# Performance work log

Hardware: AMD Instinct MI355X
Metric: run time of the kernel (lower is better)

The kernel has to match this reference:

```python
import jax, jax.numpy as jnp
import numpy as np

B, T, N, D, E = 16, 12, 512, 128, 32  # batch, time, nodes, model_dim, node_emb_dim


def setup_inputs() -> dict:
    key = jax.random.key(0)
    ks = jax.random.split(key, 7)
    return {
        "value": jax.random.normal(ks[0], (B, T, N, D), dtype=jnp.float32),
        "emb": jax.random.normal(ks[1], (T, N, E), dtype=jnp.float32),
        "attn_mask": jax.random.randint(ks[2], (B, N, N), 0, 2, dtype=jnp.int32),
        "W_qk": jax.random.normal(ks[3], (E, D), dtype=jnp.float32) * (1.0 / np.sqrt(E)),
        "b_qk": jax.random.normal(ks[4], (D,), dtype=jnp.float32) * 0.02,
        "W_v": jax.random.normal(ks[5], (D, D), dtype=jnp.float32) * (1.0 / np.sqrt(D)),
        "b_v": jax.random.normal(ks[6], (D,), dtype=jnp.float32) * 0.02,
    }


def reference(value, emb, attn_mask, W_qk, b_qk, W_v, b_v):
    # qk projection shared between query and key: [T, N, D]
    qk = emb @ W_qk + b_qk
    # query: softmax over feature dim D
    q = jax.nn.softmax(qk, axis=-1)                      # [T, N, D]
    # key: transpose then softmax over node dim N
    k = jax.nn.softmax(jnp.swapaxes(qk, -1, -2), axis=-1)  # [T, D, N]
    # value projection (note: out_proj in __init__ is unused in forward)
    v = value @ W_v + b_v                                # [B, T, N, D]
    # batch-independent base attention score, then broadcast over batch
    score = jnp.einsum('tnd,tdm->tnm', q, k)             # [T, N, N]
    score = jnp.broadcast_to(score[None], (value.shape[0],) + score.shape)  # [B, T, N, N]
    # masked fill: mask [B, N, N] -> [B, 1, N, N]
    score = jnp.where(attn_mask[:, None] == 0, jnp.float32(-1e9), score)
    out = jnp.einsum('btnm,btmd->btnd', score, v)         # [B, T, N, D]
    return out
```

## Files before the change

kernel.cpp:

```cpp
#include <hip/hip_runtime.h>

#define B_ 16
#define T_ 12
#define N_ 512
#define D_ 128
#define E_ 32

typedef __attribute__((ext_vector_type(8))) unsigned short u16x8;
typedef __attribute__((ext_vector_type(8))) __bf16 bf16x8;
typedef __attribute__((ext_vector_type(4))) float f32x4;

static __device__ __forceinline__ unsigned short f2bf(float f) {
    unsigned u = __float_as_uint(f);
    unsigned r = (u + 0x7fffu + ((u >> 16) & 1u)) >> 16;
    return (unsigned short)r;
}

static __device__ __forceinline__ void gld16(const void* src, void* dst) {
    __builtin_amdgcn_global_load_lds(
        (const __attribute__((address_space(1))) unsigned*)src,
        (__attribute__((address_space(3))) unsigned*)dst, 16, 0, 0);
}

__global__ __launch_bounds__(256) void k1(const float* __restrict__ emb,
                                          const float* __restrict__ Wqk,
                                          const float* __restrict__ bqk,
                                          unsigned short* __restrict__ qb,
                                          unsigned short* __restrict__ kN,
                                          const float* __restrict__ Wv,
                                          unsigned short* __restrict__ WvT,
                                          const int* __restrict__ mask,
                                          unsigned* __restrict__ mb) {
    __shared__ __align__(16) char LE[256 * 128];
    __shared__ float red[2][4][8];
    int bid = blockIdx.x;
    int tid = threadIdx.x;

    if (bid < 192) {
        int t = bid >> 4;
        int d0 = (bid & 15) * 8;
        int dc = tid & 7, ni = tid >> 3;
        float wqv[E_];
#pragma unroll
        for (int e = 0; e < E_; ++e) wqv[e] = Wqk[e * D_ + d0 + dc];
        float bq = bqk[d0 + dc];
        const float4* eb4 = (const float4*)(emb + (size_t)t * N_ * E_);

        float4 st0[8], st1[8];
#pragma unroll
        for (int ii = 0; ii < 8; ++ii) st0[ii] = eb4[ii * 256 + tid];
#pragma unroll
        for (int ii = 0; ii < 8; ++ii) {
            int f = ii * 256 + tid;
            int n = f >> 3, s = f & 7;
            *(float4*)(LE + n * 128 + ((s * 16) ^ ((n & 7) << 4))) = st0[ii];
        }
#pragma unroll
        for (int ii = 0; ii < 8; ++ii) st1[ii] = eb4[2048 + ii * 256 + tid];
        __syncthreads();

        float vals[16];
#pragma unroll
        for (int jj = 0; jj < 8; ++jj) {
            int n = ni + 32 * jj;
            float a = bq;
#pragma unroll
            for (int s = 0; s < 8; ++s) {
                f32x4 ev = *(const f32x4*)(LE + n * 128 + ((s * 16) ^ ((n & 7) << 4)));
                a = fmaf(ev[0], wqv[s * 4 + 0], a);
                a = fmaf(ev[1], wqv[s * 4 + 1], a);
                a = fmaf(ev[2], wqv[s * 4 + 2], a);
                a = fmaf(ev[3], wqv[s * 4 + 3], a);
            }
            vals[jj] = a;
        }
        __syncthreads();
#pragma unroll
        for (int ii = 0; ii < 8; ++ii) {
            int f = ii * 256 + tid;
            int n = f >> 3, s = f & 7;
            *(float4*)(LE + n * 128 + ((s * 16) ^ ((n & 7) << 4))) = st1[ii];
        }
        __syncthreads();
#pragma unroll
        for (int jj = 0; jj < 8; ++jj) {
            int n = ni + 32 * jj;
            float a = bq;
#pragma unroll
            for (int s = 0; s < 8; ++s) {
                f32x4 ev = *(const f32x4*)(LE + n * 128 + ((s * 16) ^ ((n & 7) << 4)));
                a = fmaf(ev[0], wqv[s * 4 + 0], a);
                a = fmaf(ev[1], wqv[s * 4 + 1], a);
                a = fmaf(ev[2], wqv[s * 4 + 2], a);
                a = fmaf(ev[3], wqv[s * 4 + 3], a);
            }
            vals[8 + jj] = a;
        }

        float mx = -1e30f;
#pragma unroll
        for (int j = 0; j < 16; ++j) mx = fmaxf(mx, vals[j]);
#pragma unroll
        for (int s = 8; s < 64; s <<= 1) mx = fmaxf(mx, __shfl_xor(mx, s));
        int wv = tid >> 6;
        if ((tid & 63) < 8) red[0][wv][dc] = mx;
        __syncthreads();
        mx = fmaxf(fmaxf(red[0][0][dc], red[0][1][dc]),
                   fmaxf(red[0][2][dc], red[0][3][dc]));
        float sum = 0.f;
#pragma unroll
        for (int j = 0; j < 16; ++j) {
            vals[j] = __expf(vals[j] - mx);
            sum += vals[j];
        }
#pragma unroll
        for (int s = 8; s < 64; s <<= 1) sum += __shfl_xor(sum, s);
        if ((tid & 63) < 8) red[1][wv][dc] = sum;
        __syncthreads();
        sum = red[1][0][dc] + red[1][1][dc] + red[1][2][dc] + red[1][3][dc];
        float inv = 1.f / sum;
        unsigned short* op = kN + (size_t)t * N_ * D_ + d0 + dc;
#pragma unroll
        for (int j = 0; j < 16; ++j)
            op[(size_t)(ni + 32 * j) * D_] = f2bf(vals[j] * inv);
        return;
    }

    if (bid < 576) {
        int bid2 = bid - 192;
        int w = tid >> 6, l = tid & 63;
        float wq0[E_], wq1[E_];
#pragma unroll
        for (int e = 0; e < E_; ++e) {
            wq0[e] = Wqk[e * D_ + l];
            wq1[e] = Wqk[e * D_ + l + 64];
        }
        float b0 = bqk[l], b1 = bqk[l + 64];
        for (int rr = 0; rr < 4; ++rr) {
            int tn = bid2 * 16 + w * 4 + rr;
            const float* ep = emb + (size_t)tn * E_;
            float a0 = b0, a1 = b1;
#pragma unroll
            for (int e = 0; e < E_; ++e) {
                float ev = ep[e];
                a0 = fmaf(ev, wq0[e], a0);
                a1 = fmaf(ev, wq1[e], a1);
            }
            float mx = fmaxf(a0, a1);
#pragma unroll
            for (int s = 32; s > 0; s >>= 1) mx = fmaxf(mx, __shfl_xor(mx, s));
            float e0 = __expf(a0 - mx), e1 = __expf(a1 - mx);
            float sum = e0 + e1;
#pragma unroll
            for (int s = 32; s > 0; s >>= 1) sum += __shfl_xor(sum, s);
            float inv = 1.f / sum;
            qb[(size_t)tn * D_ + l] = f2bf(e0 * inv);
            qb[(size_t)tn * D_ + l + 64] = f2bf(e1 * inv);
        }
        return;
    }

    if (bid < 1088) {
        int o = (bid - 576) * 256 + tid;
        const int* mp = mask + (size_t)o * 32;
        unsigned bits = 0;
#pragma unroll
        for (int j = 0; j < 32; j += 4) {
            int4 m4 = *(const int4*)&mp[j];
            bits |= (m4.x ? 1u : 0u) << j;
            bits |= (m4.y ? 1u : 0u) << (j + 1);
            bits |= (m4.z ? 1u : 0u) << (j + 2);
            bits |= (m4.w ? 1u : 0u) << (j + 3);
        }
        mb[o] = bits;
        return;
    }

    {
        int i = (bid - 1088) * 256 + tid;
        int d = i >> 7, k = i & 127;
        WvT[d * 128 + k] = f2bf(Wv[k * 128 + d]);
    }
}

__global__ __launch_bounds__(256, 2) void kF(const unsigned short* __restrict__ qb,
                                             const unsigned short* __restrict__ kN,
                                             unsigned short* __restrict__ sc,
                                             const float* __restrict__ value,
                                             const unsigned short* __restrict__ WvT,
                                             const float* __restrict__ bv,
                                             unsigned short* __restrict__ vT) {
    __shared__ __align__(16) char LA[2][128 * 128];
    __shared__ __align__(16) char LB[2][128 * 128];
    int bid = blockIdx.x;
    int tid = threadIdx.x;
    int wave = tid >> 6, lane = tid & 63;
    int q = lane >> 4, lr = lane & 15;
    int rbase = (wave & 1) * 64, cbase = (wave >> 1) * 64;
    int l3 = lane >> 3, l7 = lane & 7;

    f32x4 acc[4][4];
#pragma unroll
    for (int i = 0; i < 4; ++i)
#pragma unroll
        for (int j = 0; j < 4; ++j) acc[i][j] = (f32x4){0.f, 0.f, 0.f, 0.f};

#define STAGE_T(gbase, lb, c)                                                   \
    _Pragma("unroll") for (int it_ = 0; it_ < 4; ++it_) {                       \
        int row_ = it_ * 32 + wave * 8 + l3;                                    \
        gld16((gbase) + (size_t)row_ * 256 + (c) * 128 +                        \
                  ((l7 * 16) ^ ((row_ & 7) << 4)),                              \
              (lb) + (it_ * 32 + wave * 8) * 128 + lane * 16);                  \
    }

#define MFMA_CHUNK(c)                                                           \
    _Pragma("unroll") for (int ksl_ = 0; ksl_ < 2; ++ksl_) {                    \
        bf16x8 a_[4], b_[4];                                                    \
        _Pragma("unroll") for (int i_ = 0; i_ < 4; ++i_) {                      \
            int r_ = rbase + 16 * i_ + lr;                                      \
            a_[i_] = *(const bf16x8*)(LA[c] + r_ * 128 +                        \
                                      ((ksl_ * 64 + q * 16) ^ ((r_ & 7) << 4)));\
        }                                                                       \
        _Pragma("unroll") for (int j_ = 0; j_ < 4; ++j_) {                      \
            int r_ = cbase + 16 * j_ + lr;                                      \
            b_[j_] = *(const bf16x8*)(LB[c] + r_ * 128 +                        \
                                      ((ksl_ * 64 + q * 16) ^ ((r_ & 7) << 4)));\
        }                                                                       \
        _Pragma("unroll") for (int i_ = 0; i_ < 4; ++i_)                        \
            _Pragma("unroll") for (int j_ = 0; j_ < 4; ++j_)                    \
                acc[i_][j_] = __builtin_amdgcn_mfma_f32_16x16x32_bf16(          \
                    a_[i_], b_[j_], acc[i_][j_], 0, 0, 0);                      \
    }

    if (bid < 192) {
        int mt = bid & 3, nt = (bid >> 2) & 3, t = bid >> 4;
        int n0 = nt * 128, m0 = mt * 128;
        const char* qp = (const char*)(qb + (size_t)t * N_ * D_ + (size_t)n0 * D_);
        const char* kp = (const char*)(kN + (size_t)t * N_ * D_ + (size_t)m0 * D_);
        STAGE_T(qp, LA[0], 0)
        STAGE_T(kp, LB[0], 0)
        STAGE_T(qp, LA[1], 1)
        STAGE_T(kp, LB[1], 1)
        asm volatile("s_waitcnt vmcnt(8)" ::: "memory");
        __builtin_amdgcn_sched_barrier(0);
        __builtin_amdgcn_s_barrier();
        __builtin_amdgcn_sched_barrier(0);
        MFMA_CHUNK(0)
        asm volatile("s_waitcnt vmcnt(0)" ::: "memory");
        __builtin_amdgcn_sched_barrier(0);
        __builtin_amdgcn_s_barrier();
        __builtin_amdgcn_sched_barrier(0);
        MFMA_CHUNK(1)

        unsigned short* sp = sc + (size_t)t * N_ * N_;
#pragma unroll
        for (int i = 0; i < 4; ++i)
#pragma unroll
            for (int j = 0; j < 4; ++j) {
                int row0 = n0 + rbase + 16 * i + q * 4;
                int col = m0 + cbase + 16 * j + lr;
#pragma unroll
                for (int e = 0; e < 4; ++e)
                    sp[(size_t)(row0 + e) * N_ + col] = f2bf(acc[i][j][e]);
            }
        return;
    }

    {
        int idx = bid - 192;
        int mt = idx & 3, bt = idx >> 2;
        int m0 = mt * 128;
        const float* vp = value + ((size_t)bt * N_ + m0) * D_;
        const char* wp = (const char*)WvT;
        int g = tid >> 4, c16 = tid & 15;

        float4 v0[8], v1[8];
#pragma unroll
        for (int jj = 0; jj < 8; ++jj)
            v0[jj] = *(const float4*)(vp + (size_t)(g * 8 + jj) * D_ + c16 * 4);
        __builtin_amdgcn_sched_barrier(0);
        STAGE_T(wp, LA[0], 0)
        __builtin_amdgcn_sched_barrier(0);
#pragma unroll
        for (int jj = 0; jj < 8; ++jj)
            v1[jj] = *(const float4*)(vp + (size_t)(g * 8 + jj) * D_ + 64 + c16 * 4);
        __builtin_amdgcn_sched_barrier(0);
        STAGE_T(wp, LA[1], 1)
        __builtin_amdgcn_sched_barrier(0);

#pragma unroll
        for (int jj = 0; jj < 8; ++jj) {
            int row = g * 8 + jj;
            ushort4 o;
            o.x = f2bf(v0[jj].x); o.y = f2bf(v0[jj].y);
            o.z = f2bf(v0[jj].z); o.w = f2bf(v0[jj].w);
            *(ushort4*)(LB[0] + row * 128 + ((c16 * 8) ^ ((row & 7) << 4))) = o;
        }
        asm volatile("s_waitcnt vmcnt(12) lgkmcnt(0)" ::: "memory");
        __builtin_amdgcn_sched_barrier(0);
        __builtin_amdgcn_s_barrier();
        __builtin_amdgcn_sched_barrier(0);
        MFMA_CHUNK(0)
#pragma unroll
        for (int jj = 0; jj < 8; ++jj) {
            int row = g * 8 + jj;
            ushort4 o;
            o.x = f2bf(v1[jj].x); o.y = f2bf(v1[jj].y);
            o.z = f2bf(v1[jj].z); o.w = f2bf(v1[jj].w);
            *(ushort4*)(LB[1] + row * 128 + ((c16 * 8) ^ ((row & 7) << 4))) = o;
        }
        asm volatile("s_waitcnt vmcnt(0) lgkmcnt(0)" ::: "memory");
        __builtin_amdgcn_sched_barrier(0);
        __builtin_amdgcn_s_barrier();
        __builtin_amdgcn_sched_barrier(0);
        MFMA_CHUNK(1)

        unsigned short* op = vT + (size_t)bt * N_ * D_;
#pragma unroll
        for (int i = 0; i < 4; ++i) {
            int row0 = rbase + 16 * i + q * 4;
            float4 bq = *(const float4*)&bv[row0];
#pragma unroll
            for (int j = 0; j < 4; ++j) {
                int col = m0 + cbase + 16 * j + lr;
                op[(size_t)(row0 + 0) * N_ + col] = f2bf(acc[i][j][0] + bq.x);
                op[(size_t)(row0 + 1) * N_ + col] = f2bf(acc[i][j][1] + bq.y);
                op[(size_t)(row0 + 2) * N_ + col] = f2bf(acc[i][j][2] + bq.z);
                op[(size_t)(row0 + 3) * N_ + col] = f2bf(acc[i][j][3] + bq.w);
            }
        }
    }
#undef STAGE_T
#undef MFMA_CHUNK
}

__global__ __launch_bounds__(256, 3) void kC(const unsigned short* __restrict__ sc,
                                             const unsigned* __restrict__ mb,
                                             const unsigned short* __restrict__ vT,
                                             float* __restrict__ out) {
    int n0 = blockIdx.x * 128;
    int t = blockIdx.y, b = blockIdx.z;
    int tid = threadIdx.x;
    int wave = tid >> 6, lane = tid & 63;
    int q = lane >> 4, lr = lane & 15;
    int rbase = (wave & 1) * 64, cbase = (wave >> 1) * 64;

    __shared__ unsigned short Sb[128 * 64];
    __shared__ unsigned short Vb[2][128 * 64];

    const unsigned short* scp = sc + (size_t)t * N_ * N_ + (size_t)n0 * N_;
    const unsigned short* vtp = vT + ((size_t)(b * T_ + t)) * N_ * D_;
    const unsigned* mbp = mb + ((size_t)b * N_ + n0) * 16;
    const unsigned short NEG = 0xCE6E;

    f32x4 acc[4][4];
#pragma unroll
    for (int i = 0; i < 4; ++i)
#pragma unroll
        for (int j = 0; j < 4; ++j) acc[i][j] = (f32x4){0.f, 0.f, 0.f, 0.f};

    int sr = tid >> 1, sh2 = tid & 1;
    const unsigned short* sg = scp + (size_t)sr * N_ + sh2 * 32;
    const unsigned* mwp = mbp + sr * 16 + sh2;
    int swz_r = (sr & 7) << 4;
    char* Sw[4];
#pragma unroll
    for (int p = 0; p < 4; ++p)
        Sw[p] = (char*)Sb + sr * 128 + ((sh2 * 64 + p * 16) ^ swz_r);

    int l3 = lane >> 3, l7 = lane & 7;
    int vin = (l7 * 16) ^ (l3 << 4);
    const char* vbase = (const char*)vtp;

#pragma unroll
    for (int it = 0; it < 4; ++it) {
        int row = (it * 4 + wave) * 8 + l3;
        const char* src = vbase + (size_t)row * 1024 + vin;
        char* dst = (char*)&Vb[0][0] + ((it * 4 + wave) * 64 + lane) * 16;
        gld16(src, dst);
    }
    u16x8 sreg[4];
    unsigned mw;
#pragma unroll
    for (int p = 0; p < 4; ++p) sreg[p] = *(const u16x8*)(sg + p * 8);
    mw = mwp[0];

    for (int kc = 0; kc < 8; ++kc) {
        int cur = kc & 1;
#pragma unroll
        for (int p = 0; p < 4; ++p) {
            unsigned bits = mw >> (p * 8);
            u16x8 o;
#pragma unroll
            for (int j = 0; j < 8; ++j)
                o[j] = ((bits >> j) & 1u) ? sreg[p][j] : NEG;
            *(u16x8*)Sw[p] = o;
        }
        if (kc < 7) {
            int off = (kc + 1) * 128;
#pragma unroll
            for (int it = 0; it < 4; ++it) {
                int row = (it * 4 + wave) * 8 + l3;
                const char* src = vbase + (size_t)row * 1024 + off + vin;
                char* dst = (char*)&Vb[cur ^ 1][0] + ((it * 4 + wave) * 64 + lane) * 16;
                gld16(src, dst);
            }
            int eoff = (kc + 1) * 64;
#pragma unroll
            for (int p = 0; p < 4; ++p) sreg[p] = *(const u16x8*)(sg + eoff + p * 8);
            mw = mwp[(kc + 1) * 2];
        }
        asm volatile("s_waitcnt lgkmcnt(0)" ::: "memory");
        __builtin_amdgcn_s_barrier();
        __builtin_amdgcn_sched_barrier(0);
        {
            const char* Sbase = (const char*)Sb;
            const char* Vbase = (const char*)&Vb[cur][0];
            int swz_l = (lr & 7) << 4;
#pragma unroll
            for (int ks = 0; ks < 2; ++ks) {
                bf16x8 a[4], bb[4];
#pragma unroll
                for (int i = 0; i < 4; ++i) {
                    int r = rbase + 16 * i + lr;
                    a[i] = *(const bf16x8*)(Sbase + r * 128 + ((ks * 64 + q * 16) ^ swz_l));
                }
#pragma unroll
                for (int j = 0; j < 4; ++j) {
                    int d = cbase + 16 * j + lr;
                    bb[j] = *(const bf16x8*)(Vbase + d * 128 + ((ks * 64 + q * 16) ^ swz_l));
                }
#pragma unroll
                for (int i = 0; i < 4; ++i)
#pragma unroll
                    for (int j = 0; j < 4; ++j)
                        acc[i][j] = __builtin_amdgcn_mfma_f32_16x16x32_bf16(
                            a[i], bb[j], acc[i][j], 0, 0, 0);
            }
        }
        __builtin_amdgcn_s_barrier();
        __builtin_amdgcn_sched_barrier(0);
    }

    float* ob = out + ((size_t)(b * T_ + t)) * N_ * D_;
#pragma unroll
    for (int i = 0; i < 4; ++i) {
#pragma unroll
        for (int j = 0; j < 4; ++j) {
            int row0 = n0 + rbase + 16 * i + q * 4;
            int col = cbase + 16 * j + lr;
#pragma unroll
            for (int e = 0; e < 4; ++e)
                ob[(size_t)(row0 + e) * D_ + col] = acc[i][j][e];
        }
    }
}

extern "C" void kernel_launch(void* const* d_in, const int* in_sizes, int n_in,
                              void* d_out, int out_size, void* d_ws, size_t ws_size,
                              hipStream_t stream) {
    const float* value = (const float*)d_in[0];
    const float* emb   = (const float*)d_in[1];
    const int*   mask  = (const int*)d_in[2];
    const float* Wqk   = (const float*)d_in[3];
    const float* bqk   = (const float*)d_in[4];
    const float* Wv    = (const float*)d_in[5];
    const float* bvv   = (const float*)d_in[6];
    float* out = (float*)d_out;

    float* ws = (float*)d_ws;
    unsigned short* qb   = (unsigned short*)(ws + 786432);
    unsigned short* kNb  = (unsigned short*)(ws + 1179648);
    unsigned short* scb  = (unsigned short*)(ws + 1572864);
    unsigned short* vtb  = (unsigned short*)(ws + 3145728);
    unsigned short* WvTb = (unsigned short*)(ws + 9437184);
    unsigned*       mbp  = (unsigned*)(ws + 9445376);

    k1<<<1152, 256, 0, stream>>>(emb, Wqk, bqk, qb, kNb, Wv, WvTb, mask, mbp);
    kF<<<960, 256, 0, stream>>>(qb, kNb, scb, value, WvTb, bvv, vtb);
    kC<<<dim3(4, T_, B_), 256, 0, stream>>>(scb, mbp, vtb, out);
}
```

Before: 157.3 us.

## Remap block IDs to group work per XCD and use async LDS loads for emb

All three kernels now permute blockIdx.x so that consecutive logical blocks land on the same XCD, since hardware hands blocks out round-robin across 8 XCDs. The aim is to improve L2 reuse of the shared score and value tiles. kC moves from a 3D grid to a 1D grid so the remap can apply. In k1, the register-staged emb loads are replaced with direct global_load_lds copies done in two passes, which drops VGPR staging but serialises each load behind a barrier.

Measured after the change: 157.6 us. Within noise of the previous version (+0.2%).

```diff
diff --git a/kernel.cpp b/kernel.cpp
--- a/kernel.cpp
+++ b/kernel.cpp
@@ -33,68 +33,50 @@
                                           unsigned* __restrict__ mb) {
     __shared__ __align__(16) char LE[256 * 128];
     __shared__ float red[2][4][8];
-    int bid = blockIdx.x;
+    int hwid = blockIdx.x;
+    int bid = (hwid & 7) * 144 + (hwid >> 3);
     int tid = threadIdx.x;
 
     if (bid < 192) {
         int t = bid >> 4;
         int d0 = (bid & 15) * 8;
         int dc = tid & 7, ni = tid >> 3;
+        int wave = tid >> 6, lane = tid & 63;
+        int l3 = lane >> 3, l7 = lane & 7;
         float wqv[E_];
 #pragma unroll
         for (int e = 0; e < E_; ++e) wqv[e] = Wqk[e * D_ + d0 + dc];
         float bq = bqk[d0 + dc];
-        const float4* eb4 = (const float4*)(emb + (size_t)t * N_ * E_);
-
-        float4 st0[8], st1[8];
-#pragma unroll
-        for (int ii = 0; ii < 8; ++ii) st0[ii] = eb4[ii * 256 + tid];
-#pragma unroll
-        for (int ii = 0; ii < 8; ++ii) {
-            int f = ii * 256 + tid;
-            int n = f >> 3, s = f & 7;
-            *(float4*)(LE + n * 128 + ((s * 16) ^ ((n & 7) << 4))) = st0[ii];
-        }
-#pragma unroll
-        for (int ii = 0; ii < 8; ++ii) st1[ii] = eb4[2048 + ii * 256 + tid];
-        __syncthreads();
+        const char* eb = (const char*)(emb + (size_t)t * N_ * E_);
 
         float vals[16];
 #pragma unroll
-        for (int jj = 0; jj < 8; ++jj) {
-            int n = ni + 32 * jj;
-            float a = bq;
-#pragma unroll
-            for (int s = 0; s < 8; ++s) {
-                f32x4 ev = *(const f32x4*)(LE + n * 128 + ((s * 16) ^ ((n & 7) << 4)));
-                a = fmaf(ev[0], wqv[s * 4 + 0], a);
-                a = fmaf(ev[1], wqv[s * 4 + 1], a);
-                a = fmaf(ev[2], wqv[s * 4 + 2], a);
-                a = fmaf(ev[3], wqv[s * 4 + 3], a);
-            }
-            vals[jj] = a;
-        }
-        __syncthreads();
-#pragma unroll
-        for (int ii = 0; ii < 8; ++ii) {
-            int f = ii * 256 + tid;
-            int n = f >> 3, s = f & 7;
-            *(float4*)(LE + n * 128 + ((s * 16) ^ ((n & 7) << 4))) = st1[ii];
-        }
-        __syncthreads();
-#pragma unroll
-        for (int jj = 0; jj < 8; ++jj) {
-            int n = ni + 32 * jj;
-            float a = bq;
-#pragma unroll
-            for (int s = 0; s < 8; ++s) {
-                f32x4 ev = *(const f32x4*)(LE + n * 128 + ((s * 16) ^ ((n & 7) << 4)));
-                a = fmaf(ev[0], wqv[s * 4 + 0], a);
-                a = fmaf(ev[1], wqv[s * 4 + 1], a);
-                a = fmaf(ev[2], wqv[s * 4 + 2], a);
-                a = fmaf(ev[3], wqv[s * 4 + 3], a);
-            }
-            vals[8 + jj] = a;
+        for (int pass = 0; pass < 2; ++pass) {
+#pragma unroll
+            for (int it = 0; it < 8; ++it) {
+                int rl = it * 32 + wave * 8 + l3;
+                int rg = pass * 256 + rl;
+                gld16(eb + (size_t)rg * 128 + ((l7 * 16) ^ ((rg & 7) << 4)),
+                      LE + (it * 32 + wave * 8) * 128 + lane * 16);
+            }
+            __syncthreads();
+#pragma unroll
+            for (int jj = 0; jj < 8; ++jj) {
+                int n = pass * 256 + ni + 32 * jj;
+                int nl = ni + 32 * jj;
+                float a = bq;
+#pragma unroll
+                for (int s = 0; s < 8; ++s) {
+                    f32x4 ev = *(const f32x4*)(LE + nl * 128 +
+                                               ((s * 16) ^ ((n & 7) << 4)));
+                    a = fmaf(ev[0], wqv[s * 4 + 0], a);
+                    a = fmaf(ev[1], wqv[s * 4 + 1], a);
+                    a = fmaf(ev[2], wqv[s * 4 + 2], a);
+                    a = fmaf(ev[3], wqv[s * 4 + 3], a);
+                }
+                vals[pass * 8 + jj] = a;
+            }
+            __syncthreads();
         }
 
         float mx = -1e30f;
@@ -192,7 +174,8 @@
                                              unsigned short* __restrict__ vT) {
     __shared__ __align__(16) char LA[2][128 * 128];
     __shared__ __align__(16) char LB[2][128 * 128];
-    int bid = blockIdx.x;
+    int hwid = blockIdx.x;
+    int bid = (hwid & 7) * 120 + (hwid >> 3);
     int tid = threadIdx.x;
     int wave = tid >> 6, lane = tid & 63;
     int q = lane >> 4, lr = lane & 15;
@@ -338,8 +321,11 @@
                                              const unsigned* __restrict__ mb,
                                              const unsigned short* __restrict__ vT,
                                              float* __restrict__ out) {
-    int n0 = blockIdx.x * 128;
-    int t = blockIdx.y, b = blockIdx.z;
+    int hwid = blockIdx.x;
+    int w = (hwid & 7) * 96 + (hwid >> 3);
+    int n0 = (w & 3) * 128;
+    int r = w >> 2;
+    int t = r % T_, b = r / T_;
     int tid = threadIdx.x;
     int wave = tid >> 6, lane = tid & 63;
     int q = lane >> 4, lr = lane & 15;
@@ -422,8 +408,8 @@
                 bf16x8 a[4], bb[4];
 #pragma unroll
                 for (int i = 0; i < 4; ++i) {
-                    int r = rbase + 16 * i + lr;
-                    a[i] = *(const bf16x8*)(Sbase + r * 128 + ((ks * 64 + q * 16) ^ swz_l));
+                    int rr = rbase + 16 * i + lr;
+                    a[i] = *(const bf16x8*)(Sbase + rr * 128 + ((ks * 64 + q * 16) ^ swz_l));
                 }
 #pragma unroll
                 for (int j = 0; j < 4; ++j) {
@@ -478,5 +464,5 @@
 
     k1<<<1152, 256, 0, stream>>>(emb, Wqk, bqk, qb, kNb, Wv, WvTb, mask, mbp);
     kF<<<960, 256, 0, stream>>>(qb, kNb, scb, value, WvTb, bvv, vtb);
-    kC<<<dim3(4, T_, B_), 256, 0, stream>>>(scb, mbp, vtb, out);
-}
+    kC<<<768, 256, 0, stream>>>(scb, mbp, vtb, out);
+}
```
